# Kernel tuning notes

Measured on AMD Instinct MI355X. Metric: run time of the kernel, lower is better.

## Reference

```python
import jax, jax.numpy as jnp
import numpy as np

N_FFT = 256
HOP = 64
HS = 126  # window hop in STFT frames (hard-coded in original)


def _stft(x):
    # torch.stft(center=True, pad_mode='reflect', window=None -> rectangular,
    # onesided=True, normalized=False). x: [B, N] -> [B, T, F] (time-major,
    # matching the module's permute(0,1,3,2)).
    pad = N_FFT // 2
    xp = jnp.pad(x, ((0, 0), (pad, pad)), mode='reflect')
    T = x.shape[-1] // HOP + 1
    idx = jnp.arange(T)[:, None] * HOP + jnp.arange(N_FFT)[None, :]  # [T, n_fft]
    frames = xp[:, idx]  # [B, T, n_fft]
    return jnp.fft.rfft(frames, axis=-1)  # [B, T, F=129]


def _spec_match(mix, aux):
    mixS = _stft(mix[:, 0, :])  # [B, Tm, F] complex
    auxS = _stft(aux[:, 0, :])  # [B, Ta, F] complex
    B, Tm, F = mixS.shape
    Ta = auxS.shape[1]
    length = (Ta - Tm) // HS
    pad = HS - (Ta - Tm) % HS
    auxS = jnp.pad(auxS, ((0, 0), (0, pad), (0, 0)))
    # All sliding windows at once: [B, W, Tm, F]
    W = length + 2
    widx = jnp.arange(W)[:, None] * HS + jnp.arange(Tm)[None, :]  # [W, Tm]
    wins = auxS[:, widx, :]  # [B, W, Tm, F]
    # Real part of complex cosine similarity, elementwise
    m = mixS[:, None]  # [B, 1, Tm, F]
    sim = (m.real * wins.real + m.imag * wins.imag) / (jnp.abs(m) * jnp.abs(wins))
    flat = sim.reshape(B, W, -1)
    n = flat.shape[-1]
    # torch.median = lower median; torch.median returns NaN if any NaN present
    srt = jnp.sort(flat, axis=-1)
    med = srt[..., (n - 1) // 2]
    med = jnp.where(jnp.isnan(flat).any(-1), -jnp.inf, med)
    best = jnp.argmax(med, axis=1)  # [B], first max like Python max()
    sel = jnp.take_along_axis(wins, best[:, None, None, None], axis=1)  # [B,1,Tm,F]
    return jnp.concatenate([sel.real, sel.imag], axis=1)  # [B, 2, Tm, F]


def setup_inputs() -> dict:
    key = jax.random.key(0)
    k1, k2 = jax.random.split(key)
    mix = jax.random.normal(k1, (8, 1, 65536), dtype=jnp.float32)
    aux = jax.random.normal(k2, (8, 1, 262144), dtype=jnp.float32)
    return {"mix": mix, "aux": aux}


def reference(mix, aux):
    return _spec_match(mix, aux)
```

## Files before the change

### kernel.cpp

```cpp
#include <hip/hip_runtime.h>
#include <math.h>

constexpr int NFFT  = 256;
constexpr int HOP   = 64;
constexpr int NBIN  = 129;
constexpr int NB    = 8;
constexpr int LMIX  = 65536;
constexpr int LAUX  = 262144;
constexpr int TM    = 1025;
constexpr int TA    = 4097;
constexpr int TROWS = 4175;
constexpr int HS    = 126;
constexpr int W     = 26;
constexpr int NJOBS = NB * W;
constexpr int NVAL  = TM * NBIN;
constexpr int KMED  = (NVAL - 1) / 2;
constexpr int CHUNKS = 8;

constexpr size_t MIXN_OFF  = 0;
constexpr size_t MIXN_BYTES = (size_t)NB * TM * NBIN * sizeof(float2);
constexpr size_t AUXN_OFF  = MIXN_OFF + MIXN_BYTES;
constexpr size_t AUXN_BYTES = (size_t)NB * TROWS * NBIN * sizeof(float2);
constexpr size_t HIST_OFF  = AUXN_OFF + AUXN_BYTES;
constexpr size_t HIST_BYTES = (size_t)NJOBS * CHUNKS * 2048 * 4;
constexpr size_t CAND_OFF  = HIST_OFF + HIST_BYTES;
constexpr size_t CAND_BYTES = (size_t)NJOBS * NVAL * 4;
constexpr size_t TW_OFF    = CAND_OFF + CAND_BYTES;
constexpr size_t TW_BYTES  = 256 * sizeof(float2);
constexpr size_t NAN_OFF   = TW_OFF + TW_BYTES;
constexpr size_t NCAND_OFF = NAN_OFF + 832;
constexpr size_t SELBIN_OFF= NCAND_OFF + 832;
constexpr size_t KREM_OFF  = SELBIN_OFF + 832;
constexpr size_t MED_OFF   = KREM_OFF + 832;
constexpr size_t BEST_OFF  = MED_OFF + 832;

__global__ void build_table(float2* __restrict__ tw, unsigned* __restrict__ nanC,
                            unsigned* __restrict__ ncand)
{
    int i = threadIdx.x;
    double ang = (double)i * (-2.0 * 3.14159265358979323846 / 256.0);
    tw[i] = make_float2((float)cos(ang), (float)sin(ang));
    if (i < NJOBS) { nanC[i] = 0u; ncand[i] = 0u; }
}

template<int FPB, bool NORM>
__global__ void stft_fft(const float* __restrict__ x, const float2* __restrict__ twg,
                         int L, int Tframes, int Trows, float2* __restrict__ out)
{
    constexpr int NX = 64 * (FPB - 1) + NFFT;
    __shared__ float  xs[NX];
    __shared__ float2 Y[FPB][16][16];
    __shared__ float2 cis16[16];

    const int tid = threadIdx.x;
    const int b   = blockIdx.y;
    const int f0  = blockIdx.x * FPB;

    if (tid < 16) cis16[tid] = twg[(16 * tid) & 255];

    for (int i = tid; i < NX; i += 256) {
        int j = f0 * HOP + i - 128;
        if (j < 0) j = -j;
        if (j >= L) j = 2 * L - 2 - j;
        xs[i] = x[(size_t)b * L + j];
    }
    __syncthreads();

    const int n1 = (tid >> 4) & 15;
    const int r  = tid & 15;
    #pragma unroll
    for (int f = 0; f < FPB; ++f) {
        float re = 0.f, im = 0.f;
        int idx = 0;
        #pragma unroll
        for (int n2 = 0; n2 < 16; ++n2) {
            float  v = xs[f * HOP + n1 + 16 * n2];
            float2 t = cis16[idx];
            re = fmaf(v, t.x, re);
            im = fmaf(v, t.y, im);
            idx = (idx + r) & 15;
        }
        Y[f][n1][r] = make_float2(re, im);
    }
    __syncthreads();

    const float QNAN = __int_as_float(0x7FC00000);
    for (int jj = tid; jj < FPB * NBIN; jj += 256) {
        int f  = jj / NBIN;
        int k  = jj - f * NBIN;
        int fr = f0 + f;
        if (fr >= Trows) continue;
        float2 o;
        if (fr < Tframes) {
            float2 dk = twg[k];
            float tr = 1.f, ti = 0.f;
            float ar = 0.f, ai = 0.f;
            #pragma unroll
            for (int s = 0; s < 16; ++s) {
                float2 y = Y[f][s][k & 15];
                ar = fmaf(tr, y.x, ar); ar = fmaf(-ti, y.y, ar);
                ai = fmaf(tr, y.y, ai); ai = fmaf( ti, y.x, ai);
                float nr = tr * dk.x - ti * dk.y;
                ti = fmaf(tr, dk.y, ti * dk.x);
                tr = nr;
            }
            if (NORM) {
                float inv = rsqrtf(ar * ar + ai * ai);
                o = make_float2(ar * inv, ai * inv);
            } else {
                o = make_float2(ar, ai);
            }
        } else {
            o = NORM ? make_float2(QNAN, QNAN) : make_float2(0.f, 0.f);
        }
        out[((size_t)b * Trows + fr) * NBIN + k] = o;
    }
}

__device__ __forceinline__ unsigned flip_key(float s) {
    unsigned u = __float_as_uint(s);
    return (u & 0x80000000u) ? ~u : (u | 0x80000000u);
}

__device__ __forceinline__ unsigned qbin(float s) {
    if (!(s == s)) return 2047u;
    int bq = (int)floorf(fmaf(s, 1024.f, 1024.f));
    bq = max(0, min(2047, bq));
    return (unsigned)bq;
}

template<int PER>
__device__ __forceinline__ void rank_find(const unsigned (&bins)[PER], unsigned target,
                                          unsigned& out_bin, unsigned& out_rem)
{
    __shared__ unsigned wtot[4];
    __shared__ unsigned result[2];
    const int tid  = threadIdx.x;
    const int lane = tid & 63;
    const int wid  = tid >> 6;

    unsigned st = 0;
    #pragma unroll
    for (int i = 0; i < PER; ++i) st += bins[i];

    unsigned inc = st;
    #pragma unroll
    for (int d = 1; d < 64; d <<= 1) {
        unsigned v = __shfl_up(inc, d);
        if (lane >= d) inc += v;
    }
    if (lane == 63) wtot[wid] = inc;
    __syncthreads();

    unsigned wbase = 0;
    for (int wme = 0; wme < wid; ++wme) wbase += wtot[wme];
    unsigned ex = wbase + inc - st;
    bool pred = (ex <= target) && (target < ex + st);
    if (pred) {
        unsigned cum = ex;
        #pragma unroll
        for (int i = 0; i < PER; ++i) {
            if (cum + bins[i] > target) {
                result[0] = (unsigned)(tid * PER + i);
                result[1] = target - cum;
                break;
            }
            cum += bins[i];
        }
    }
    __syncthreads();
    out_bin = result[0];
    out_rem = result[1];
}

__global__ void sim_hist(const float2* __restrict__ mixN, const float2* __restrict__ auxN,
                         unsigned* __restrict__ hist, unsigned* __restrict__ nanCnt)
{
    constexpr int NCOPY   = 2;
    constexpr int HSTRIDE = 2049;
    __shared__ unsigned lh[NCOPY * HSTRIDE];
    const int tid   = threadIdx.x;
    const int chunk = blockIdx.x;
    const int job   = blockIdx.y;
    const int b = job / W;
    const int w = job - b * W;
    unsigned* lhc = lh + ((tid >> 4) & (NCOPY - 1)) * HSTRIDE;

    for (int i = tid; i < NCOPY * HSTRIDE; i += 256) lh[i] = 0;
    __syncthreads();

    unsigned localnan = 0;
    const float2* mrow = mixN + (size_t)b * TM * NBIN;
    const float2* arow = auxN + ((size_t)b * TROWS + (size_t)w * HS) * NBIN;

    const int pad = b & 1;
    const int lim = pad + ((NVAL - pad) & ~1);

    for (int i = pad + (chunk * 256 + tid) * 2; i < lim; i += CHUNKS * 512) {
        float4 mv = *reinterpret_cast<const float4*>(mrow + i);
        float4 av = *reinterpret_cast<const float4*>(arow + i);
        float s0 = fmaf(mv.x, av.x, mv.y * av.y);
        float s1 = fmaf(mv.z, av.z, mv.w * av.w);
        if (!(s0 == s0)) localnan++;
        if (!(s1 == s1)) localnan++;
        atomicAdd(&lhc[qbin(s0)], 1u);
        atomicAdd(&lhc[qbin(s1)], 1u);
    }
    if (chunk == 0 && tid == 0) {
        int ie = pad ? 0 : NVAL - 1;
        float2 m = mrow[ie];
        float2 a = arow[ie];
        float s = fmaf(m.x, a.x, m.y * a.y);
        if (!(s == s)) localnan++;
        atomicAdd(&lhc[qbin(s)], 1u);
    }
    __syncthreads();

    unsigned* gh = hist + ((size_t)job * CHUNKS + chunk) * 2048;
    for (int i = tid; i < 2048; i += 256) gh[i] = lh[i] + lh[HSTRIDE + i];
    if (localnan) atomicAdd(&nanCnt[job], localnan);
}

__global__ void scan_bins(const unsigned* __restrict__ hist, unsigned* __restrict__ selbin,
                          unsigned* __restrict__ krem)
{
    constexpr int PER = 8;
    const int tid = threadIdx.x;
    const int job = blockIdx.x;
    const unsigned* h = hist + (size_t)job * CHUNKS * 2048;

    unsigned bins[PER];
    #pragma unroll
    for (int i = 0; i < PER; ++i) {
        unsigned v = 0;
        int bin = tid * PER + i;
        #pragma unroll
        for (int c = 0; c < CHUNKS; ++c) v += h[(size_t)c * 2048 + bin];
        bins[i] = v;
    }

    unsigned sb, rem;
    rank_find<PER>(bins, (unsigned)KMED, sb, rem);
    if (tid == 0) { selbin[job] = sb; krem[job] = rem; }
}

__global__ void sim_compact(const float2* __restrict__ mixN, const float2* __restrict__ auxN,
                            const unsigned* __restrict__ selbin, unsigned* __restrict__ cand,
                            unsigned* __restrict__ ncand)
{
    const int tid   = threadIdx.x;
    const int chunk = blockIdx.x;
    const int job   = blockIdx.y;
    const int b = job / W;
    const int w = job - b * W;
    const unsigned sb = selbin[job];
    unsigned* candj  = cand + (size_t)job * NVAL;
    unsigned* ncandj = ncand + job;
    const int lane = tid & 63;

    const float2* mrow = mixN + (size_t)b * TM * NBIN;
    const float2* arow = auxN + ((size_t)b * TROWS + (size_t)w * HS) * NBIN;

    const int pad = b & 1;
    const int lim = pad + ((NVAL - pad) & ~1);

    for (int i = pad + (chunk * 256 + tid) * 2; i < lim; i += CHUNKS * 512) {
        float4 mv = *reinterpret_cast<const float4*>(mrow + i);
        float4 av = *reinterpret_cast<const float4*>(arow + i);
        float sv[2];
        sv[0] = fmaf(mv.x, av.x, mv.y * av.y);
        sv[1] = fmaf(mv.z, av.z, mv.w * av.w);
        #pragma unroll
        for (int u = 0; u < 2; ++u) {
            bool pred = (qbin(sv[u]) == sb);
            unsigned long long m = __ballot(pred);
            if (m) {
                int leader = __ffsll(m) - 1;
                unsigned base = 0;
                if (lane == leader) base = atomicAdd(ncandj, (unsigned)__popcll(m));
                base = (unsigned)__shfl((int)base, leader);
                if (pred) candj[base + __popcll(m & ((1ull << lane) - 1ull))] = flip_key(sv[u]);
            }
        }
    }
    if (chunk == 0 && tid == 0) {
        int ie = pad ? 0 : NVAL - 1;
        float2 m = mrow[ie];
        float2 a = arow[ie];
        float s = fmaf(m.x, a.x, m.y * a.y);
        if (qbin(s) == sb) {
            unsigned idx = atomicAdd(ncandj, 1u);
            candj[idx] = flip_key(s);
        }
    }
}

__global__ void select_kernel(const unsigned* __restrict__ cand, const unsigned* __restrict__ ncand,
                              const unsigned* __restrict__ krem, const unsigned* __restrict__ nanCnt,
                              float* __restrict__ med)
{
    __shared__ unsigned h[2048];
    const int job = blockIdx.x;
    const int tid = threadIdx.x;
    const unsigned* c = cand + (size_t)job * NVAL;
    const unsigned n = ncand[job];
    unsigned pref = 0, tgt = krem[job];

    for (int ph = 0; ph < 3; ++ph) {
        for (int i = tid; i < 2048; i += 256) h[i] = 0;
        __syncthreads();
        for (unsigned i = tid; i < n; i += 256) {
            unsigned k = c[i];
            if (ph == 0) atomicAdd(&h[k >> 21], 1u);
            else if (ph == 1) { if ((k >> 21) == (pref >> 21)) atomicAdd(&h[(k >> 10) & 2047u], 1u); }
            else { if ((k >> 10) == (pref >> 10)) atomicAdd(&h[k & 1023u], 1u); }
        }
        __syncthreads();

        unsigned bins[8];
        #pragma unroll
        for (int i = 0; i < 8; ++i) bins[i] = h[tid * 8 + i];
        unsigned sb, rem;
        rank_find<8>(bins, tgt, sb, rem);

        if (ph == 0)      pref = sb << 21;
        else if (ph == 1) pref |= sb << 10;
        else              pref |= sb;
        tgt = rem;
        __syncthreads();
    }

    if (tid == 0) {
        unsigned key = pref;
        unsigned u = (key & 0x80000000u) ? (key ^ 0x80000000u) : ~key;
        med[job] = (nanCnt[job] > 0u) ? -INFINITY : __uint_as_float(u);
    }
}

__global__ void argmax_kernel(const float* __restrict__ med, int* __restrict__ best)
{
    int b = threadIdx.x;
    if (b < NB) {
        float mx = -INFINITY; int bi = 0;
        for (int w = 0; w < W; ++w) {
            float v = med[b * W + w];
            if (v > mx) { mx = v; bi = w; }
        }
        best[b] = bi;
    }
}

template<int FPB>
__global__ void gather_stft(const float* __restrict__ x, const float2* __restrict__ twg,
                            const int* __restrict__ best, float* __restrict__ out)
{
    constexpr int NX = 64 * (FPB - 1) + NFFT;
    __shared__ float  xs[NX];
    __shared__ float2 Y[FPB][16][16];
    __shared__ float2 cis16[16];

    const int tid = threadIdx.x;
    const int b   = blockIdx.y;
    const int t0  = blockIdx.x * FPB;
    const int fr0 = best[b] * HS + t0;

    if (tid < 16) cis16[tid] = twg[(16 * tid) & 255];

    for (int i = tid; i < NX; i += 256) {
        int j = fr0 * HOP + i - 128;
        if (j < 0) j = -j;
        if (j >= LAUX) j = 2 * LAUX - 2 - j;
        j = max(0, min(LAUX - 1, j));
        xs[i] = x[(size_t)b * LAUX + j];
    }
    __syncthreads();

    const int n1 = (tid >> 4) & 15;
    const int r  = tid & 15;
    #pragma unroll
    for (int f = 0; f < FPB; ++f) {
        float re = 0.f, im = 0.f;
        int idx = 0;
        #pragma unroll
        for (int n2 = 0; n2 < 16; ++n2) {
            float  v = xs[f * HOP + n1 + 16 * n2];
            float2 t = cis16[idx];
            re = fmaf(v, t.x, re);
            im = fmaf(v, t.y, im);
            idx = (idx + r) & 15;
        }
        Y[f][n1][r] = make_float2(re, im);
    }
    __syncthreads();

    for (int jj = tid; jj < FPB * NBIN; jj += 256) {
        int f  = jj / NBIN;
        int k  = jj - f * NBIN;
        int t  = t0 + f;
        if (t >= TM) continue;
        float ar = 0.f, ai = 0.f;
        if (fr0 + f < TA) {
            float2 dk = twg[k];
            float tr = 1.f, ti = 0.f;
            #pragma unroll
            for (int s = 0; s < 16; ++s) {
                float2 y = Y[f][s][k & 15];
                ar = fmaf(tr, y.x, ar); ar = fmaf(-ti, y.y, ar);
                ai = fmaf(tr, y.y, ai); ai = fmaf( ti, y.x, ai);
                float nr = tr * dk.x - ti * dk.y;
                ti = fmaf(tr, dk.y, ti * dk.x);
                tr = nr;
            }
        }
        size_t o = (size_t)t * NBIN + k;
        out[(size_t)(b * 2 + 0) * NVAL + o] = ar;
        out[(size_t)(b * 2 + 1) * NVAL + o] = ai;
    }
}

extern "C" void kernel_launch(void* const* d_in, const int* in_sizes, int n_in,
                              void* d_out, int out_size, void* d_ws, size_t ws_size,
                              hipStream_t stream)
{
    const float* mix = (const float*)d_in[0];
    const float* aux = (const float*)d_in[1];
    float* out = (float*)d_out;
    char* ws = (char*)d_ws;

    float2*   mixN = (float2*)(ws + MIXN_OFF);
    float2*   auxN = (float2*)(ws + AUXN_OFF);
    unsigned* hist = (unsigned*)(ws + HIST_OFF);
    unsigned* cand = (unsigned*)(ws + CAND_OFF);
    float2*   twg  = (float2*)(ws + TW_OFF);
    unsigned* nanC = (unsigned*)(ws + NAN_OFF);
    unsigned* ncand= (unsigned*)(ws + NCAND_OFF);
    unsigned* selb = (unsigned*)(ws + SELBIN_OFF);
    unsigned* krem = (unsigned*)(ws + KREM_OFF);
    float*    med  = (float*)(ws + MED_OFF);
    int*      best = (int*)(ws + BEST_OFF);

    build_table<<<1, 256, 0, stream>>>(twg, nanC, ncand);

    constexpr int FPB = 4;
    stft_fft<FPB, true><<<dim3((TM + FPB - 1) / FPB, NB), 256, 0, stream>>>(mix, twg, LMIX, TM, TM, mixN);
    stft_fft<FPB, true><<<dim3((TROWS + FPB - 1) / FPB, NB), 256, 0, stream>>>(aux, twg, LAUX, TA, TROWS, auxN);

    sim_hist<<<dim3(CHUNKS, NJOBS), 256, 0, stream>>>(mixN, auxN, hist, nanC);
    scan_bins<<<NJOBS, 256, 0, stream>>>(hist, selb, krem);
    sim_compact<<<dim3(CHUNKS, NJOBS), 256, 0, stream>>>(mixN, auxN, selb, cand, ncand);
    select_kernel<<<NJOBS, 256, 0, stream>>>(cand, ncand, krem, nanC, med);

    argmax_kernel<<<1, 64, 0, stream>>>(med, best);
    gather_stft<FPB><<<dim3((TM + FPB - 1) / FPB, NB), 256, 0, stream>>>(aux, twg, best, out);
}
```

Baseline: 133.8 us.

## Fuse pipeline stages to cut kernel launches and shrink the histogram

Merges the mix and aux STFTs into one launch and drops the twiddle-table kernel in favour of on-the-fly sincosf. The bin scan moves into sim_compact and the argmax into gather_stft, and NaN counts are written per chunk instead of by global atomic. The histogram shrinks from 2048 to 1024 bins with four privatized copies, and the STFT output loop is unrolled two-wide. This removes four kernel launches and their serialization gaps. In exchange, each compact block redoes the histogram reduction, and coarser bins mean more candidates in the selection stage.

```diff
diff --git a/kernel.cpp b/kernel.cpp
--- a/kernel.cpp
+++ b/kernel.cpp
@@ -16,36 +16,34 @@
 constexpr int NVAL  = TM * NBIN;
 constexpr int KMED  = (NVAL - 1) / 2;
 constexpr int CHUNKS = 8;
+constexpr int NBA   = 1024;
+constexpr int FPB   = 4;
+constexpr int MIXBLKS = (TM + FPB - 1) / FPB;
+constexpr int AUXBLKS = (TROWS + FPB - 1) / FPB;
 
 constexpr size_t MIXN_OFF  = 0;
 constexpr size_t MIXN_BYTES = (size_t)NB * TM * NBIN * sizeof(float2);
 constexpr size_t AUXN_OFF  = MIXN_OFF + MIXN_BYTES;
 constexpr size_t AUXN_BYTES = (size_t)NB * TROWS * NBIN * sizeof(float2);
 constexpr size_t HIST_OFF  = AUXN_OFF + AUXN_BYTES;
-constexpr size_t HIST_BYTES = (size_t)NJOBS * CHUNKS * 2048 * 4;
+constexpr size_t HIST_BYTES = (size_t)NJOBS * CHUNKS * NBA * 4;
 constexpr size_t CAND_OFF  = HIST_OFF + HIST_BYTES;
 constexpr size_t CAND_BYTES = (size_t)NJOBS * NVAL * 4;
-constexpr size_t TW_OFF    = CAND_OFF + CAND_BYTES;
-constexpr size_t TW_BYTES  = 256 * sizeof(float2);
-constexpr size_t NAN_OFF   = TW_OFF + TW_BYTES;
-constexpr size_t NCAND_OFF = NAN_OFF + 832;
-constexpr size_t SELBIN_OFF= NCAND_OFF + 832;
-constexpr size_t KREM_OFF  = SELBIN_OFF + 832;
+constexpr size_t NAN_OFF   = CAND_OFF + CAND_BYTES;
+constexpr size_t NAN_BYTES = (size_t)NJOBS * CHUNKS * 4;
+constexpr size_t NCAND_OFF = NAN_OFF + NAN_BYTES;
+constexpr size_t KREM_OFF  = NCAND_OFF + 832;
 constexpr size_t MED_OFF   = KREM_OFF + 832;
-constexpr size_t BEST_OFF  = MED_OFF + 832;
-
-__global__ void build_table(float2* __restrict__ tw, unsigned* __restrict__ nanC,
-                            unsigned* __restrict__ ncand)
-{
-    int i = threadIdx.x;
-    double ang = (double)i * (-2.0 * 3.14159265358979323846 / 256.0);
-    tw[i] = make_float2((float)cos(ang), (float)sin(ang));
-    if (i < NJOBS) { nanC[i] = 0u; ncand[i] = 0u; }
-}
-
-template<int FPB, bool NORM>
-__global__ void stft_fft(const float* __restrict__ x, const float2* __restrict__ twg,
-                         int L, int Tframes, int Trows, float2* __restrict__ out)
+
+__device__ __forceinline__ float2 twiddle(int k) {
+    float s, c;
+    sincosf((float)(-2.0 * 3.14159265358979323846 / 256.0) * (float)k, &s, &c);
+    return make_float2(c, s);
+}
+
+__global__ void stft_all(const float* __restrict__ mix, const float* __restrict__ aux,
+                         float2* __restrict__ mixN, float2* __restrict__ auxN,
+                         unsigned* __restrict__ ncand)
 {
     constexpr int NX = 64 * (FPB - 1) + NFFT;
     __shared__ float  xs[NX];
@@ -54,9 +52,18 @@
 
     const int tid = threadIdx.x;
     const int b   = blockIdx.y;
-    const int f0  = blockIdx.x * FPB;
-
-    if (tid < 16) cis16[tid] = twg[(16 * tid) & 255];
+    const int bx  = blockIdx.x;
+    const bool isMix = bx < MIXBLKS;
+    const int f0 = (isMix ? bx : bx - MIXBLKS) * FPB;
+    const int L       = isMix ? LMIX : LAUX;
+    const int Tframes = isMix ? TM : TA;
+    const int Trows   = isMix ? TM : TROWS;
+    const float* x    = isMix ? mix : aux;
+    float2* out       = isMix ? mixN : auxN;
+
+    if (bx == 0 && b == 0 && tid < NJOBS) ncand[tid] = 0u;
+
+    if (tid < 16) cis16[tid] = twiddle(16 * tid);
 
     for (int i = tid; i < NX; i += 256) {
         int j = f0 * HOP + i - 128;
@@ -85,35 +92,56 @@
     __syncthreads();
 
     const float QNAN = __int_as_float(0x7FC00000);
-    for (int jj = tid; jj < FPB * NBIN; jj += 256) {
-        int f  = jj / NBIN;
-        int k  = jj - f * NBIN;
-        int fr = f0 + f;
-        if (fr >= Trows) continue;
+    auto emit = [&](int fr, int k, float ar, float ai) {
+        if (fr >= Trows) return;
         float2 o;
         if (fr < Tframes) {
-            float2 dk = twg[k];
-            float tr = 1.f, ti = 0.f;
-            float ar = 0.f, ai = 0.f;
-            #pragma unroll
-            for (int s = 0; s < 16; ++s) {
-                float2 y = Y[f][s][k & 15];
-                ar = fmaf(tr, y.x, ar); ar = fmaf(-ti, y.y, ar);
-                ai = fmaf(tr, y.y, ai); ai = fmaf( ti, y.x, ai);
-                float nr = tr * dk.x - ti * dk.y;
-                ti = fmaf(tr, dk.y, ti * dk.x);
-                tr = nr;
-            }
-            if (NORM) {
-                float inv = rsqrtf(ar * ar + ai * ai);
-                o = make_float2(ar * inv, ai * inv);
-            } else {
-                o = make_float2(ar, ai);
-            }
+            float inv = rsqrtf(ar * ar + ai * ai);
+            o = make_float2(ar * inv, ai * inv);
         } else {
-            o = NORM ? make_float2(QNAN, QNAN) : make_float2(0.f, 0.f);
+            o = make_float2(QNAN, QNAN);
         }
         out[((size_t)b * Trows + fr) * NBIN + k] = o;
+    };
+
+    {
+        const int jjA = tid, jjB = tid + 256;
+        const int fA = jjA / NBIN, kA = jjA - fA * NBIN;
+        const int fB = jjB / NBIN, kB = jjB - fB * NBIN;
+        const float2 dkA = twiddle(kA);
+        const float2 dkB = twiddle(kB);
+        float trA = 1.f, tiA = 0.f, arA = 0.f, aiA = 0.f;
+        float trB = 1.f, tiB = 0.f, arB = 0.f, aiB = 0.f;
+        #pragma unroll
+        for (int s = 0; s < 16; ++s) {
+            float2 yA = Y[fA][s][kA & 15];
+            float2 yB = Y[fB][s][kB & 15];
+            arA = fmaf(trA, yA.x, arA); arA = fmaf(-tiA, yA.y, arA);
+            aiA = fmaf(trA, yA.y, aiA); aiA = fmaf( tiA, yA.x, aiA);
+            arB = fmaf(trB, yB.x, arB); arB = fmaf(-tiB, yB.y, arB);
+            aiB = fmaf(trB, yB.y, aiB); aiB = fmaf( tiB, yB.x, aiB);
+            float nrA = trA * dkA.x - tiA * dkA.y;
+            tiA = fmaf(trA, dkA.y, tiA * dkA.x); trA = nrA;
+            float nrB = trB * dkB.x - tiB * dkB.y;
+            tiB = fmaf(trB, dkB.y, tiB * dkB.x); trB = nrB;
+        }
+        emit(f0 + fA, kA, arA, aiA);
+        emit(f0 + fB, kB, arB, aiB);
+    }
+    if (tid < FPB * NBIN - 512) {
+        const int jj = 512 + tid;
+        const int f = jj / NBIN, k = jj - f * NBIN;
+        const float2 dk = twiddle(k);
+        float tr = 1.f, ti = 0.f, ar = 0.f, ai = 0.f;
+        #pragma unroll
+        for (int s = 0; s < 16; ++s) {
+            float2 y = Y[f][s][k & 15];
+            ar = fmaf(tr, y.x, ar); ar = fmaf(-ti, y.y, ar);
+            ai = fmaf(tr, y.y, ai); ai = fmaf( ti, y.x, ai);
+            float nr = tr * dk.x - ti * dk.y;
+            ti = fmaf(tr, dk.y, ti * dk.x); tr = nr;
+        }
+        emit(f0 + f, k, ar, ai);
     }
 }
 
@@ -123,9 +151,9 @@
 }
 
 __device__ __forceinline__ unsigned qbin(float s) {
-    if (!(s == s)) return 2047u;
-    int bq = (int)floorf(fmaf(s, 1024.f, 1024.f));
-    bq = max(0, min(2047, bq));
+    if (!(s == s)) return (unsigned)(NBA - 1);
+    int bq = (int)floorf(fmaf(s, 512.f, 512.f));
+    bq = max(0, min(NBA - 1, bq));
     return (unsigned)bq;
 }
 
@@ -155,8 +183,7 @@
     unsigned wbase = 0;
     for (int wme = 0; wme < wid; ++wme) wbase += wtot[wme];
     unsigned ex = wbase + inc - st;
-    bool pred = (ex <= target) && (target < ex + st);
-    if (pred) {
+    if ((ex <= target) && (target < ex + st)) {
         unsigned cum = ex;
         #pragma unroll
         for (int i = 0; i < PER; ++i) {
@@ -176,9 +203,10 @@
 __global__ void sim_hist(const float2* __restrict__ mixN, const float2* __restrict__ auxN,
                          unsigned* __restrict__ hist, unsigned* __restrict__ nanCnt)
 {
-    constexpr int NCOPY   = 2;
-    constexpr int HSTRIDE = 2049;
+    constexpr int NCOPY   = 4;
+    constexpr int HSTRIDE = NBA + 1;
     __shared__ unsigned lh[NCOPY * HSTRIDE];
+    __shared__ unsigned bnan;
     const int tid   = threadIdx.x;
     const int chunk = blockIdx.x;
     const int job   = blockIdx.y;
@@ -187,6 +215,7 @@
     unsigned* lhc = lh + ((tid >> 4) & (NCOPY - 1)) * HSTRIDE;
 
     for (int i = tid; i < NCOPY * HSTRIDE; i += 256) lh[i] = 0;
+    if (tid == 0) bnan = 0;
     __syncthreads();
 
     unsigned localnan = 0;
@@ -214,46 +243,39 @@
         if (!(s == s)) localnan++;
         atomicAdd(&lhc[qbin(s)], 1u);
     }
-    __syncthreads();
-
-    unsigned* gh = hist + ((size_t)job * CHUNKS + chunk) * 2048;
-    for (int i = tid; i < 2048; i += 256) gh[i] = lh[i] + lh[HSTRIDE + i];
-    if (localnan) atomicAdd(&nanCnt[job], localnan);
-}
-
-__global__ void scan_bins(const unsigned* __restrict__ hist, unsigned* __restrict__ selbin,
-                          unsigned* __restrict__ krem)
-{
-    constexpr int PER = 8;
-    const int tid = threadIdx.x;
-    const int job = blockIdx.x;
-    const unsigned* h = hist + (size_t)job * CHUNKS * 2048;
-
-    unsigned bins[PER];
-    #pragma unroll
-    for (int i = 0; i < PER; ++i) {
-        unsigned v = 0;
-        int bin = tid * PER + i;
-        #pragma unroll
-        for (int c = 0; c < CHUNKS; ++c) v += h[(size_t)c * 2048 + bin];
-        bins[i] = v;
-    }
-
-    unsigned sb, rem;
-    rank_find<PER>(bins, (unsigned)KMED, sb, rem);
-    if (tid == 0) { selbin[job] = sb; krem[job] = rem; }
+    if (localnan) atomicAdd(&bnan, localnan);
+    __syncthreads();
+
+    unsigned* gh = hist + ((size_t)job * CHUNKS + chunk) * NBA;
+    for (int i = tid; i < NBA; i += 256)
+        gh[i] = lh[i] + lh[HSTRIDE + i] + lh[2 * HSTRIDE + i] + lh[3 * HSTRIDE + i];
+    if (tid == 0) nanCnt[job * CHUNKS + chunk] = bnan;
 }
 
 __global__ void sim_compact(const float2* __restrict__ mixN, const float2* __restrict__ auxN,
-                            const unsigned* __restrict__ selbin, unsigned* __restrict__ cand,
-                            unsigned* __restrict__ ncand)
+                            const unsigned* __restrict__ hist, unsigned* __restrict__ cand,
+                            unsigned* __restrict__ ncand, unsigned* __restrict__ krem)
 {
     const int tid   = threadIdx.x;
     const int chunk = blockIdx.x;
     const int job   = blockIdx.y;
     const int b = job / W;
     const int w = job - b * W;
-    const unsigned sb = selbin[job];
+
+    unsigned bins[NBA / 256];
+    const unsigned* h = hist + (size_t)job * CHUNKS * NBA;
+    #pragma unroll
+    for (int i = 0; i < NBA / 256; ++i) {
+        unsigned v = 0;
+        int bin = tid * (NBA / 256) + i;
+        #pragma unroll
+        for (int c = 0; c < CHUNKS; ++c) v += h[(size_t)c * NBA + bin];
+        bins[i] = v;
+    }
+    unsigned sb, rem;
+    rank_find<NBA / 256>(bins, (unsigned)KMED, sb, rem);
+    if (chunk == 0 && tid == 0) krem[job] = rem;
+
     unsigned* candj  = cand + (size_t)job * NVAL;
     unsigned* ncandj = ncand + job;
     const int lane = tid & 63;
@@ -331,40 +353,40 @@
     }
 
     if (tid == 0) {
+        unsigned nan = 0;
+        #pragma unroll
+        for (int c2 = 0; c2 < CHUNKS; ++c2) nan += nanCnt[job * CHUNKS + c2];
         unsigned key = pref;
         unsigned u = (key & 0x80000000u) ? (key ^ 0x80000000u) : ~key;
-        med[job] = (nanCnt[job] > 0u) ? -INFINITY : __uint_as_float(u);
-    }
-}
-
-__global__ void argmax_kernel(const float* __restrict__ med, int* __restrict__ best)
-{
-    int b = threadIdx.x;
-    if (b < NB) {
+        med[job] = (nan > 0u) ? -INFINITY : __uint_as_float(u);
+    }
+}
+
+__global__ void gather_stft(const float* __restrict__ x, const float* __restrict__ med,
+                            float* __restrict__ out)
+{
+    constexpr int NX = 64 * (FPB - 1) + NFFT;
+    __shared__ float  xs[NX];
+    __shared__ float2 Y[FPB][16][16];
+    __shared__ float2 cis16[16];
+    __shared__ int sh_best;
+
+    const int tid = threadIdx.x;
+    const int b   = blockIdx.y;
+    const int t0  = blockIdx.x * FPB;
+
+    if (tid == 0) {
         float mx = -INFINITY; int bi = 0;
         for (int w = 0; w < W; ++w) {
             float v = med[b * W + w];
             if (v > mx) { mx = v; bi = w; }
         }
-        best[b] = bi;
-    }
-}
-
-template<int FPB>
-__global__ void gather_stft(const float* __restrict__ x, const float2* __restrict__ twg,
-                            const int* __restrict__ best, float* __restrict__ out)
-{
-    constexpr int NX = 64 * (FPB - 1) + NFFT;
-    __shared__ float  xs[NX];
-    __shared__ float2 Y[FPB][16][16];
-    __shared__ float2 cis16[16];
-
-    const int tid = threadIdx.x;
-    const int b   = blockIdx.y;
-    const int t0  = blockIdx.x * FPB;
-    const int fr0 = best[b] * HS + t0;
-
-    if (tid < 16) cis16[tid] = twg[(16 * tid) & 255];
+        sh_best = bi;
+    }
+    if (tid < 16) cis16[tid] = twiddle(16 * tid);
+    __syncthreads();
+
+    const int fr0 = sh_best * HS + t0;
 
     for (int i = tid; i < NX; i += 256) {
         int j = fr0 * HOP + i - 128;
@@ -400,7 +422,7 @@
         if (t >= TM) continue;
         float ar = 0.f, ai = 0.f;
         if (fr0 + f < TA) {
-            float2 dk = twg[k];
+            float2 dk = twiddle(k);
             float tr = 1.f, ti = 0.f;
             #pragma unroll
             for (int s = 0; s < 16; ++s) {
@@ -431,25 +453,14 @@
     float2*   auxN = (float2*)(ws + AUXN_OFF);
     unsigned* hist = (unsigned*)(ws + HIST_OFF);
     unsigned* cand = (unsigned*)(ws + CAND_OFF);
-    float2*   twg  = (float2*)(ws + TW_OFF);
     unsigned* nanC = (unsigned*)(ws + NAN_OFF);
     unsigned* ncand= (unsigned*)(ws + NCAND_OFF);
-    unsigned* selb = (unsigned*)(ws + SELBIN_OFF);
     unsigned* krem = (unsigned*)(ws + KREM_OFF);
     float*    med  = (float*)(ws + MED_OFF);
-    int*      best = (int*)(ws + BEST_OFF);
-
-    build_table<<<1, 256, 0, stream>>>(twg, nanC, ncand);
-
-    constexpr int FPB = 4;
-    stft_fft<FPB, true><<<dim3((TM + FPB - 1) / FPB, NB), 256, 0, stream>>>(mix, twg, LMIX, TM, TM, mixN);
-    stft_fft<FPB, true><<<dim3((TROWS + FPB - 1) / FPB, NB), 256, 0, stream>>>(aux, twg, LAUX, TA, TROWS, auxN);
-
+
+    stft_all<<<dim3(MIXBLKS + AUXBLKS, NB), 256, 0, stream>>>(mix, aux, mixN, auxN, ncand);
     sim_hist<<<dim3(CHUNKS, NJOBS), 256, 0, stream>>>(mixN, auxN, hist, nanC);
-    scan_bins<<<NJOBS, 256, 0, stream>>>(hist, selb, krem);
-    sim_compact<<<dim3(CHUNKS, NJOBS), 256, 0, stream>>>(mixN, auxN, selb, cand, ncand);
+    sim_compact<<<dim3(CHUNKS, NJOBS), 256, 0, stream>>>(mixN, auxN, hist, cand, ncand, krem);
     select_kernel<<<NJOBS, 256, 0, stream>>>(cand, ncand, krem, nanC, med);
-
-    argmax_kernel<<<1, 64, 0, stream>>>(med, best);
-    gather_stft<FPB><<<dim3((TM + FPB - 1) / FPB, NB), 256, 0, stream>>>(aux, twg, best, out);
-}
+    gather_stft<<<dim3((TM + FPB - 1) / FPB, NB), 256, 0, stream>>>(aux, med, out);
+}
```

Result: slower. 136.5 us (+2.0%).
